# Optimization experiments

Hardware: AMD Instinct MI355X
Metric: run time of the kernel (lower is better)

The kernel has to match this reference:

```python
import jax, jax.numpy as jnp
import numpy as np

EMB = 1024
HEADS = 16
DH = EMB // HEADS
EPS = 1e-5


def _layernorm(x, w, b):
    mean = jnp.mean(x, axis=-1, keepdims=True)
    var = jnp.mean((x - mean) ** 2, axis=-1, keepdims=True)  # unbiased=False
    return w * (x - mean) / jnp.sqrt(var + EPS) + b


def _gelu_tanh(x):
    c = jnp.sqrt(jnp.asarray(2.0 / jnp.pi, x.dtype))
    return 0.5 * x * (1.0 + jnp.tanh(c * (x + 0.044715 * x ** 3)))


def setup_inputs() -> dict:
    key = jax.random.key(0)
    ks = jax.random.split(key, 8)
    B, N = 2, 2048
    s = lambda fan_in: 1.0 / np.sqrt(fan_in)
    # weights stored as [in, out] (torch Linear applied as x @ W.T == x @ W_here)
    return {
        "x": jax.random.normal(ks[0], (B, N, EMB), jnp.float32),
        "ln1_w": jnp.ones((EMB,), jnp.float32),
        "ln1_b": jnp.zeros((EMB,), jnp.float32),
        "w_qkv": jax.random.normal(ks[1], (EMB, 3 * EMB), jnp.float32) * s(EMB),  # qkv_bias=False
        "w_attn_proj": jax.random.normal(ks[2], (EMB, EMB), jnp.float32) * s(EMB),
        "b_attn_proj": jnp.zeros((EMB,), jnp.float32),
        "ln2_w": jnp.ones((EMB,), jnp.float32),
        "ln2_b": jnp.zeros((EMB,), jnp.float32),
        "w_fc": jax.random.normal(ks[3], (EMB, 4 * EMB), jnp.float32) * s(EMB),
        "b_fc": jnp.zeros((4 * EMB,), jnp.float32),
        "w_proj": jax.random.normal(ks[4], (4 * EMB, EMB), jnp.float32) * s(4 * EMB),
        "b_proj": jnp.zeros((EMB,), jnp.float32),
    }


def reference(x, ln1_w, ln1_b, w_qkv, w_attn_proj, b_attn_proj,
              ln2_w, ln2_b, w_fc, b_fc, w_proj, b_proj):
    B, N, _ = x.shape
    # --- attention sublayer (pre-LN) ---
    h = _layernorm(x, ln1_w, ln1_b)
    qkv = h @ w_qkv  # [B,N,3E]
    q, k, v = jnp.split(qkv, 3, axis=-1)
    # [B,H,N,Dh]
    q = q.reshape(B, N, HEADS, DH).transpose(0, 2, 1, 3)
    k = k.reshape(B, N, HEADS, DH).transpose(0, 2, 1, 3)
    v = v.reshape(B, N, HEADS, DH).transpose(0, 2, 1, 3)
    scores = jnp.einsum("bhqd,bhkd->bhqk", q, k) * (DH ** -0.5)
    causal = jnp.tril(jnp.ones((N, N), bool))
    scores = jnp.where(causal, scores, -jnp.inf)
    attn = jax.nn.softmax(scores, axis=-1)  # attn_pdrop=0 (eval)
    ctx = jnp.einsum("bhqk,bhkd->bhqd", attn, v)
    ctx = ctx.transpose(0, 2, 1, 3).reshape(B, N, EMB)
    x = x + (ctx @ w_attn_proj + b_attn_proj)  # resid_pdrop=0
    # --- MLP sublayer (pre-LN) ---
    h = _layernorm(x, ln2_w, ln2_b)
    h = _gelu_tanh(h @ w_fc + b_fc)
    x = x + (h @ w_proj + b_proj)
    return x
```

## Files before the change

### kernel.cpp

```cpp
#include <hip/hip_runtime.h>
#include <stdint.h>

#define EMB 1024
#define NHEAD 16
#define DH 64
#define SEQ 2048
#define NTOK 4096

typedef __attribute__((ext_vector_type(8))) short s16x8;
typedef __attribute__((ext_vector_type(4))) short s16x4;
typedef __attribute__((ext_vector_type(4))) float f32x4;
typedef __attribute__((ext_vector_type(4))) unsigned short u16x4;

__device__ __forceinline__ unsigned short f2bf(float f){
    union { float f; unsigned int u; } v; v.f = f;
    unsigned int r = v.u + 0x7fffu + ((v.u >> 16) & 1u);
    return (unsigned short)(r >> 16);
}

__device__ __forceinline__ f32x4 mfma16(s16x8 a, s16x8 b, f32x4 c){
    return __builtin_amdgcn_mfma_f32_16x16x32_bf16(a, b, c, 0, 0, 0);
}

__device__ __forceinline__ void gload16(const void* g, void* l){
    __builtin_amdgcn_global_load_lds((const __attribute__((address_space(1))) void*)g,
                                     (__attribute__((address_space(3))) void*)l, 16, 0, 0);
}

__device__ __forceinline__ s16x8 cat8(s16x4 a, s16x4 b){
    s16x8 r;
    r[0]=a[0]; r[1]=a[1]; r[2]=a[2]; r[3]=a[3];
    r[4]=b[0]; r[5]=b[1]; r[6]=b[2]; r[7]=b[3];
    return r;
}

__device__ __forceinline__ unsigned cvtpk(float lo, float hi){
    unsigned r;
    asm("v_cvt_pk_bf16_f32 %0, %1, %2" : "=v"(r) : "v"(lo), "v"(hi));
    return r;
}

__device__ __forceinline__ s16x8 qscale(s16x8 q){
    s16x8 r;
    #pragma unroll
    for (int e = 0; e < 8; ++e){
        union { float f; unsigned u; } v;
        v.u = ((unsigned)(unsigned short)q[e]) << 16;
        v.f *= 0.125f;
        r[e] = (short)f2bf(v.f);
    }
    return r;
}

__global__ __launch_bounds__(256) void convT_kernel(const float* __restrict__ in,
                                                    unsigned short* __restrict__ out,
                                                    int R, int C){
    __shared__ float tile[32][33];
    const int c0 = blockIdx.x * 32, r0 = blockIdx.y * 32;
    const int tx = threadIdx.x, ty = threadIdx.y;
    #pragma unroll
    for (int k = 0; k < 4; ++k)
        tile[ty*4+k][tx] = in[(long)(r0 + ty*4 + k) * C + c0 + tx];
    __syncthreads();
    #pragma unroll
    for (int k = 0; k < 4; ++k)
        out[(long)(c0 + ty*4 + k) * R + r0 + tx] = f2bf(tile[tx][ty*4+k]);
}

__global__ __launch_bounds__(256) void vT_kernel(const unsigned short* __restrict__ qkv,
                                                 unsigned short* __restrict__ vtg){
    __shared__ unsigned short tile[64*64];
    const int bh = blockIdx.y, b = bh >> 4, h = bh & 15;
    const int n0 = blockIdx.x * 64;
    const int t = threadIdx.x;
    const int nr = t >> 3, c0 = (t & 7) * 8;
    #pragma unroll
    for (int hh = 0; hh < 2; ++hh){
        const int n = nr + hh*32;
        uint4 vv = *(const uint4*)&qkv[(long)(b*SEQ + n0 + n)*3072 + 2048 + h*64 + c0];
        *(uint4*)((char*)tile + n*128 + ((c0*2) ^ (((n>>3)&7)<<4))) = vv;
    }
    __syncthreads();
    #pragma unroll
    for (int hh = 0; hh < 2; ++hh){
        const int d = nr + hh*32;
        union { unsigned short u[8]; uint4 v; } tmp;
        #pragma unroll
        for (int j = 0; j < 8; ++j){
            const int n = c0 + j;
            tmp.u[j] = *(const unsigned short*)((char*)tile + n*128 + ((d*2) ^ (((n>>3)&7)<<4)));
        }
        *(uint4*)&vtg[((long)bh*64 + d)*2048 + n0 + c0] = tmp.v;
    }
}

__global__ __launch_bounds__(256) void ln_kernel(const float* __restrict__ x,
                                                 const float* __restrict__ w,
                                                 const float* __restrict__ b,
                                                 unsigned short* __restrict__ out){
    const int row = blockIdx.x, tid = threadIdx.x;
    const float4 v = ((const float4*)(x + (long)row * EMB))[tid];
    float s  = v.x + v.y + v.z + v.w;
    float ss = v.x*v.x + v.y*v.y + v.z*v.z + v.w*v.w;
    #pragma unroll
    for (int off = 32; off >= 1; off >>= 1){
        s  += __shfl_xor(s,  off, 64);
        ss += __shfl_xor(ss, off, 64);
    }
    __shared__ float ps[4], pss[4];
    const int wv = tid >> 6;
    if ((tid & 63) == 0){ ps[wv] = s; pss[wv] = ss; }
    __syncthreads();
    s  = ps[0] + ps[1] + ps[2] + ps[3];
    ss = pss[0] + pss[1] + pss[2] + pss[3];
    const float mean = s * (1.0f/EMB);
    const float var  = ss * (1.0f/EMB) - mean*mean;
    const float rstd = rsqrtf(var + 1e-5f);
    const float4 wv4 = ((const float4*)w)[tid];
    const float4 bv4 = ((const float4*)b)[tid];
    u16x4 o;
    o[0] = f2bf((v.x - mean) * rstd * wv4.x + bv4.x);
    o[1] = f2bf((v.y - mean) * rstd * wv4.y + bv4.y);
    o[2] = f2bf((v.z - mean) * rstd * wv4.z + bv4.z);
    o[3] = f2bf((v.w - mean) * rstd * wv4.w + bv4.w);
    *(u16x4*)(out + (long)row * EMB + tid * 4) = o;
}

__global__ __launch_bounds__(256) void red_kernel(const float* __restrict__ p0,
                                                  const float* __restrict__ p1,
                                                  const float* __restrict__ bias,
                                                  const float* __restrict__ resid,
                                                  float* __restrict__ out, int N){
    const long i = ((long)blockIdx.x * 256 + threadIdx.x) * 4;
    const float4 a = *(const float4*)(p0 + i);
    const float4 b = *(const float4*)(p1 + i);
    const float4 r = *(const float4*)(resid + i);
    const float4 bb = *(const float4*)(bias + ((int)i & (N - 1)));
    float4 o;
    o.x = a.x + b.x + r.x + bb.x;
    o.y = a.y + b.y + r.y + bb.y;
    o.z = a.z + b.z + r.z + bb.z;
    o.w = a.w + b.w + r.w + bb.w;
    *(float4*)(out + i) = o;
}

template<int EPI, int SK>
__global__ __launch_bounds__(256, 2) void gemm4_kernel(const unsigned short* __restrict__ A,
                                                       const unsigned short* __restrict__ Bt,
                                                       const float* __restrict__ bias,
                                                       void* __restrict__ out0,
                                                       void* __restrict__ out1,
                                                       int M, int N, int K,
                                                       int xr, int yr){
    __shared__ unsigned short As[2][128*64];
    __shared__ unsigned short Bs[2][128*64];
    const int tid = threadIdx.x, lane = tid & 63, w = tid >> 6;
    const int lm = lane & 15, g = lane >> 4;
    const int wr = w >> 1, wc = w & 1;

    const int gx = gridDim.x;
    const int o = blockIdx.y * gx + blockIdx.x;
    const int x = o & 7, j = o >> 3;
    const int nrx = gx / xr;
    const int m0 = ((x / nrx) * yr + j / xr) * 128;
    const int n0 = ((x % nrx) * xr + j % xr) * 128;
    const int kz = (SK > 1) ? blockIdx.z : 0;
    const int kbase = kz * (K / SK);
    const int nkt = (K / SK) / 64;

    const int r8 = tid >> 3;
    const int src = (((tid & 7) * 16) ^ ((r8 & 7) << 4)) >> 1;
    char* AsB = (char*)&As[0][0];
    char* BsB = (char*)&Bs[0][0];

    auto stage = [&](int bu, int kt){
        #pragma unroll
        for (int p = 0; p < 4; ++p)
            gload16(&A[(long)(m0 + p*32 + r8) * K + kt + src], AsB + bu*16384 + p*4096 + tid*16);
        #pragma unroll
        for (int p = 0; p < 4; ++p)
            gload16(&Bt[(long)(n0 + p*32 + r8) * K + kt + src], BsB + bu*16384 + p*4096 + tid*16);
    };

    f32x4 zero = {0.0f, 0.0f, 0.0f, 0.0f};
    f32x4 acc[4][4];
    #pragma unroll
    for (int i = 0; i < 4; ++i)
        #pragma unroll
        for (int jj = 0; jj < 4; ++jj) acc[i][jj] = zero;

    stage(0, kbase);
    int cur = 0;
    const int axor = (lm & 7) << 4;
    for (int t = 0; t < nkt; ++t){
        if (t + 1 < nkt){
            stage(cur ^ 1, kbase + (t + 1) * 64);
            asm volatile("s_waitcnt vmcnt(8)" ::: "memory");
        } else {
            asm volatile("s_waitcnt vmcnt(0)" ::: "memory");
        }
        __builtin_amdgcn_s_barrier();
        asm volatile("" ::: "memory");
        const char* Ab = AsB + cur*16384;
        const char* Bb = BsB + cur*16384;
        #pragma unroll
        for (int kk = 0; kk < 2; ++kk){
            s16x8 af[4], bf[4];
            #pragma unroll
            for (int i = 0; i < 4; ++i)
                af[i] = *(const s16x8*)(Ab + (wr*64 + i*16 + lm)*128 + ((kk*64 + g*16) ^ axor));
            #pragma unroll
            for (int jj = 0; jj < 4; ++jj)
                bf[jj] = *(const s16x8*)(Bb + (wc*64 + jj*16 + lm)*128 + ((kk*64 + g*16) ^ axor));
            asm volatile("s_waitcnt lgkmcnt(0)" ::: "memory");
            __builtin_amdgcn_sched_barrier(0);
            __builtin_amdgcn_s_setprio(1);
            #pragma unroll
            for (int i = 0; i < 4; ++i)
                #pragma unroll
                for (int jj = 0; jj < 4; ++jj)
                    acc[i][jj] = mfma16(bf[jj], af[i], acc[i][jj]);
            __builtin_amdgcn_s_setprio(0);
        }
        asm volatile("" ::: "memory");
        __builtin_amdgcn_s_barrier();
        asm volatile("" ::: "memory");
        cur ^= 1;
    }

    float* po = (SK > 1 && kz == 1) ? (float*)out1 : (float*)out0;
    #pragma unroll
    for (int i = 0; i < 4; ++i){
        const int row = m0 + wr*64 + i*16 + lm;
        #pragma unroll
        for (int jj = 0; jj < 4; ++jj){
            const int col = n0 + wc*64 + jj*16 + 4*g;
            const f32x4 v = acc[i][jj];
            if (EPI == 0){
                u16x4 ov;
                ov[0] = f2bf(v[0]); ov[1] = f2bf(v[1]);
                ov[2] = f2bf(v[2]); ov[3] = f2bf(v[3]);
                *(u16x4*)&((unsigned short*)out0)[(long)row * N + col] = ov;
            } else if (EPI == 2){
                u16x4 ov;
                #pragma unroll
                for (int r = 0; r < 4; ++r){
                    const float xx = v[r] + bias[col + r];
                    const float z = 0.7978845608f * (xx + 0.044715f * xx * xx * xx);
                    ov[r] = f2bf(xx / (1.0f + __expf(-2.0f * z)));
                }
                *(u16x4*)&((unsigned short*)out0)[(long)row * N + col] = ov;
            } else {
                *(float4*)&po[(long)row * N + col] = *(const float4*)&v;
            }
        }
    }
}

template<int EPI, int BM, int BN, int WR, int WC, int SK>
__global__ __launch_bounds__(WR*WC*64) void gemm_kernel(const unsigned short* __restrict__ A,
                                                        const unsigned short* __restrict__ Bt,
                                                        const float* __restrict__ bias,
                                                        const float* __restrict__ resid,
                                                        void* __restrict__ out0,
                                                        void* __restrict__ out1,
                                                        int M, int N, int K){
    constexpr int NW = WR * WC;
    constexpr int NT = NW * 64;
    constexpr int FI = BM / (WR * 16);
    constexpr int FJ = BN / (WC * 16);
    __shared__ unsigned short As[2][BM * 32];
    __shared__ unsigned short Bs[2][BN * 32];
    const int tid  = threadIdx.x;
    const int lane = tid & 63, w = tid >> 6;
    const int lm = lane & 15, g = lane >> 4;
    const int wr = w / WC, wc = w % WC;

    const int gx = gridDim.x;
    const int nwg = gx * gridDim.y;
    int id = blockIdx.y * gx + blockIdx.x;
    id = (id & 7) * (nwg >> 3) + (id >> 3);
    const int m0 = (id / gx) * BM, n0 = (id % gx) * BN;
    const int kz = (SK > 1) ? blockIdx.z : 0;
    const int kbase = kz * (K / SK);

    f32x4 zero = {0.0f, 0.0f, 0.0f, 0.0f};
    f32x4 acc[FI][FJ];
    #pragma unroll
    for (int i = 0; i < FI; ++i)
        #pragma unroll
        for (int j = 0; j < FJ; ++j) acc[i][j] = zero;

    auto stage = [&](int kt, int bu){
        #pragma unroll
        for (int p = 0; p < BM/(NT/4); ++p)
            gload16(&A[(long)(m0 + p*(NT/4) + (tid>>2)) * K + kt + (tid&3)*8],
                    (char*)&As[bu][0] + p*(NT*16) + tid*16);
        #pragma unroll
        for (int p = 0; p < BN/(NT/4); ++p)
            gload16(&Bt[(long)(n0 + p*(NT/4) + (tid>>2)) * K + kt + (tid&3)*8],
                    (char*)&Bs[bu][0] + p*(NT*16) + tid*16);
    };

    stage(kbase, 0);
    int cur = 0;
    const int nkt = (K / SK) / 32;
    for (int t = 0; t < nkt; ++t){
        __syncthreads();
        if (t + 1 < nkt) stage(kbase + (t+1)*32, cur ^ 1);
        s16x8 af[FI], bf[FJ];
        #pragma unroll
        for (int i = 0; i < FI; ++i)
            af[i] = *(const s16x8*)&As[cur][(wr*(FI*16) + i*16 + lm)*32 + g*8];
        #pragma unroll
        for (int j = 0; j < FJ; ++j)
            bf[j] = *(const s16x8*)&Bs[cur][(wc*(FJ*16) + j*16 + lm)*32 + g*8];
        #pragma unroll
        for (int i = 0; i < FI; ++i)
            #pragma unroll
            for (int j = 0; j < FJ; ++j)
                acc[i][j] = mfma16(af[i], bf[j], acc[i][j]);
        cur ^= 1;
    }

    float* po = (SK > 1 && kz == 1) ? (float*)out1 : (float*)out0;
    #pragma unroll
    for (int i = 0; i < FI; ++i){
        #pragma unroll
        for (int r = 0; r < 4; ++r){
            const int row = m0 + wr*(FI*16) + i*16 + 4*g + r;
            #pragma unroll
            for (int j = 0; j < FJ; ++j){
                const int col = n0 + wc*(FJ*16) + j*16 + lm;
                const float v = acc[i][j][r];
                if (EPI == 0){
                    ((unsigned short*)out0)[(long)row * N + col] = f2bf(v);
                } else if (EPI == 1){
                    ((float*)out0)[(long)row * N + col] =
                        v + bias[col] + resid[(long)row * N + col];
                } else if (EPI == 2){
                    const float xx = v + bias[col];
                    const float z = 0.7978845608f * (xx + 0.044715f * xx * xx * xx);
                    const float gg = xx / (1.0f + __expf(-2.0f * z));
                    ((unsigned short*)out0)[(long)row * N + col] = f2bf(gg);
                } else {
                    po[(long)row * N + col] = v;
                }
            }
        }
    }
}

__global__ __launch_bounds__(256) void attn_kernel(const unsigned short* __restrict__ qkv,
                                                   const unsigned short* __restrict__ vtg,
                                                   unsigned short* __restrict__ ctx){
    __shared__ unsigned short Ks[3][4096];
    __shared__ unsigned short Vs[3][4096];
    int id0 = blockIdx.y * 16 + blockIdx.x;
    const int id = (id0 & 7) * 64 + (id0 >> 3);
    const int pair = id & 15, bh = id >> 4;
    const int b = bh >> 4, h = bh & 15;
    const int tid = threadIdx.x, lane = tid & 63, w = tid >> 6;
    const int lm = lane & 15, g = lane >> 4;
    const long qkvb = (long)b * SEQ * 3072;
    const unsigned short* kglob = qkv + qkvb + 1024 + h*64;
    const unsigned short* vglob = vtg + (long)bh * 64 * 2048;

    const int srow = tid >> 3;
    const int soff = (tid & 7) * 16;
    const int swz = (lm & 7) << 4;
    f32x4 zero = {0.0f, 0.0f, 0.0f, 0.0f};

    #pragma unroll 1
    for (int grp = 0; grp < 2; ++grp){
        const int qg = (grp == 0) ? pair : (31 - pair);
        const int q0 = qg * 64;
        const int nt = qg + 1;
        const int qrow = q0 + w*16 + lm;

        const unsigned short* qrp = qkv + qkvb + (long)qrow*3072 + h*64;
        const s16x8 qf0 = qscale(*(const s16x8*)(qrp + g*8));
        const s16x8 qf1 = qscale(*(const s16x8*)(qrp + 32 + g*8));

        f32x4 o[4];
        #pragma unroll
        for (int d = 0; d < 4; ++d) o[d] = zero;
        float lsum = 0.0f;

        auto stageKV = [&](int t, int bu){
            const int kv0 = t * 64;
            #pragma unroll
            for (int hh = 0; hh < 2; ++hh){
                const int row = srow + hh*32;
                const int sw  = soff ^ ((row & 7) << 4);
                gload16(kglob + (long)(kv0 + row)*3072 + (sw >> 1),
                        (char*)&Ks[bu][0] + hh*4096 + w*1024);
                gload16(vglob + (long)row*2048 + kv0 + (sw >> 1),
                        (char*)&Vs[bu][0] + hh*4096 + w*1024);
            }
        };
        auto qkt = [&](int bu, f32x4* sc){
            const char* Kb = (const char*)&Ks[bu][0];
            #pragma unroll
            for (int s = 0; s < 4; ++s){
                const char* rp = Kb + (s*16 + lm)*128;
                s16x8 kf0 = *(const s16x8*)(rp + ((g*16) ^ swz));
                s16x8 kf1 = *(const s16x8*)(rp + ((64 + g*16) ^ swz));
                f32x4 a = mfma16(kf0, qf0, zero);
                sc[s] = mfma16(kf1, qf1, a);
            }
        };

        __builtin_amdgcn_s_barrier();
        asm volatile("" ::: "memory");
        stageKV(0, 0);
        if (nt > 1){
            stageKV(1, 1);
            asm volatile("s_waitcnt vmcnt(4)" ::: "memory");
        } else {
            asm volatile("s_waitcnt vmcnt(0)" ::: "memory");
        }
        __builtin_amdgcn_s_barrier();
        asm volatile("" ::: "memory");

        f32x4 sc[4], scN[4];
        qkt(0, sc);

        #pragma unroll 1
        for (int t = 0; t < nt; ++t){
            const bool more = (t + 1 < nt);
            if (more){
                asm volatile("s_waitcnt vmcnt(0)" ::: "memory");
                __builtin_amdgcn_s_barrier();
                asm volatile("" ::: "memory");
                if (t + 2 < nt) stageKV(t + 2, (t + 2) % 3);
                qkt((t + 1) % 3, scN);
            }

            if (t == nt - 1){
                #pragma unroll
                for (int s = 0; s < 4; ++s)
                    #pragma unroll
                    for (int r = 0; r < 4; ++r)
                        if (s*16 + 4*g + r > w*16 + lm) sc[s][r] = -1e30f;
            }
            float pp[4][4];
            #pragma unroll
            for (int s = 0; s < 4; ++s)
                #pragma unroll
                for (int r = 0; r < 4; ++r){
                    const float e = __expf(sc[s][r]);
                    pp[s][r] = e;
                    lsum += e;
                }

            union { unsigned u[4]; s16x8 v; } P0, P1;
            P0.u[0] = cvtpk(pp[0][0], pp[0][1]);
            P0.u[1] = cvtpk(pp[0][2], pp[0][3]);
            P0.u[2] = cvtpk(pp[1][0], pp[1][1]);
            P0.u[3] = cvtpk(pp[1][2], pp[1][3]);
            P1.u[0] = cvtpk(pp[2][0], pp[2][1]);
            P1.u[1] = cvtpk(pp[2][2], pp[2][3]);
            P1.u[2] = cvtpk(pp[3][0], pp[3][1]);
            P1.u[3] = cvtpk(pp[3][2], pp[3][3]);

            const char* Vb = (const char*)&Vs[t % 3][0];
            #pragma unroll
            for (int d = 0; d < 4; ++d){
                const char* vrp = Vb + (d*16 + lm)*128;
                s16x4 a0 = *(const s16x4*)(vrp + ((g*8) ^ swz));
                s16x4 a1 = *(const s16x4*)(vrp + ((32 + g*8) ^ swz));
                o[d] = mfma16(cat8(a0, a1), P0.v, o[d]);
                s16x4 b0 = *(const s16x4*)(vrp + ((64 + g*8) ^ swz));
                s16x4 b1 = *(const s16x4*)(vrp + ((96 + g*8) ^ swz));
                o[d] = mfma16(cat8(b0, b1), P1.v, o[d]);
            }
            if (more){
                #pragma unroll
                for (int s4 = 0; s4 < 4; ++s4) sc[s4] = scN[s4];
            }
        }

        lsum += __shfl_xor(lsum, 16, 64);
        lsum += __shfl_xor(lsum, 32, 64);
        const float inv = 1.0f / lsum;
        unsigned short* cw = ctx + (long)(b*SEQ + qrow)*EMB + h*DH + 4*g;
        #pragma unroll
        for (int d = 0; d < 4; ++d){
            u16x4 ov;
            ov[0] = f2bf(o[d][0]*inv); ov[1] = f2bf(o[d][1]*inv);
            ov[2] = f2bf(o[d][2]*inv); ov[3] = f2bf(o[d][3]*inv);
            *(u16x4*)(cw + d*16) = ov;
        }
    }
}

extern "C" void kernel_launch(void* const* d_in, const int* in_sizes, int n_in,
                              void* d_out, int out_size, void* d_ws, size_t ws_size,
                              hipStream_t stream){
    const float* x     = (const float*)d_in[0];
    const float* ln1_w = (const float*)d_in[1];
    const float* ln1_b = (const float*)d_in[2];
    const float* w_qkv = (const float*)d_in[3];
    const float* w_ap  = (const float*)d_in[4];
    const float* b_ap  = (const float*)d_in[5];
    const float* ln2_w = (const float*)d_in[6];
    const float* ln2_b = (const float*)d_in[7];
    const float* w_fc  = (const float*)d_in[8];
    const float* b_fc  = (const float*)d_in[9];
    const float* w_pr  = (const float*)d_in[10];
    const float* b_pr  = (const float*)d_in[11];
    float* out = (float*)d_out;

    char* ws = (char*)d_ws;
    unsigned short* wqkvT = (unsigned short*)(ws + 0);
    unsigned short* wapT  = (unsigned short*)(ws + 6291456);
    unsigned short* wfcT  = (unsigned short*)(ws + 8388608);
    unsigned short* wprT  = (unsigned short*)(ws + 16777216);
    unsigned short* h1    = (unsigned short*)(ws + 25165824);
    unsigned short* vtg   = (unsigned short*)(ws + 25165824);
    unsigned short* qkv   = (unsigned short*)(ws + 33554432);
    unsigned short* ctx   = (unsigned short*)(ws + 58720256);
    float*          x1    = (float*)(ws + 67108864);
    unsigned short* h2    = (unsigned short*)(ws + 83886080);
    unsigned short* afc   = (unsigned short*)(ws + 92274688);
    float* pp0 = (float*)(ws + 0);
    float* pp1 = (float*)(ws + 25165824);

    dim3 b32(32, 8, 1);
    convT_kernel<<<dim3(3072/32, 1024/32), b32, 0, stream>>>(w_qkv, wqkvT, 1024, 3072);
    convT_kernel<<<dim3(1024/32, 1024/32), b32, 0, stream>>>(w_ap,  wapT,  1024, 1024);
    convT_kernel<<<dim3(4096/32, 1024/32), b32, 0, stream>>>(w_fc,  wfcT,  1024, 4096);
    convT_kernel<<<dim3(1024/32, 4096/32), b32, 0, stream>>>(w_pr,  wprT,  4096, 1024);

    ln_kernel<<<NTOK, 256, 0, stream>>>(x, ln1_w, ln1_b, h1);

    gemm4_kernel<0,1><<<dim3(3072/128, NTOK/128), 256, 0, stream>>>(
        h1, wqkvT, nullptr, qkv, nullptr, NTOK, 3072, 1024, 12, 8);

    vT_kernel<<<dim3(SEQ/64, 32), 256, 0, stream>>>(qkv, vtg);

    attn_kernel<<<dim3(16, 32), 256, 0, stream>>>(qkv, vtg, ctx);

    gemm_kernel<1,128,64,2,2,1><<<dim3(1024/64, NTOK/128), 256, 0, stream>>>(
        ctx, wapT, b_ap, x, x1, nullptr, NTOK, 1024, 1024);

    ln_kernel<<<NTOK, 256, 0, stream>>>(x1, ln2_w, ln2_b, h2);

    gemm4_kernel<2,1><<<dim3(4096/128, NTOK/128), 256, 0, stream>>>(
        h2, wfcT, b_fc, afc, nullptr, NTOK, 4096, 1024, 16, 8);

    gemm4_kernel<3,2><<<dim3(1024/128, NTOK/128, 2), 256, 0, stream>>>(
        afc, wprT, nullptr, pp0, pp1, NTOK, 1024, 4096, 8, 4);
    red_kernel<<<NTOK*EMB/1024, 256, 0, stream>>>(pp0, pp1, b_pr, x1, out, EMB);
}
```

Measured before the change: 241.2 us.

## Replace split-K proj GEMM and old attn-proj GEMM with fused 128x64 kernel

Adds a new 128x64-tile GEMM kernel that uses the swizzled 64-wide K staging, with bias and residual fused into its epilogue. It is used for both the attention output projection and the MLP down-projection. This drops the split-K partial buffers and the separate reduction kernel, and replaces the older 32-K-step GEMM. The four weight-transpose launches are also merged into one kernel. The MLP projection loses split-K parallelism but gets more blocks through the smaller N tile and an occupancy hint of 3.

```diff
diff --git a/kernel.cpp b/kernel.cpp
--- a/kernel.cpp
+++ b/kernel.cpp
@@ -52,11 +52,18 @@
     return r;
 }
 
-__global__ __launch_bounds__(256) void convT_kernel(const float* __restrict__ in,
-                                                    unsigned short* __restrict__ out,
-                                                    int R, int C){
+__global__ __launch_bounds__(256) void convT4_kernel(const float* __restrict__ q, unsigned short* __restrict__ qo,
+                                                     const float* __restrict__ a, unsigned short* __restrict__ ao,
+                                                     const float* __restrict__ f, unsigned short* __restrict__ fo,
+                                                     const float* __restrict__ p, unsigned short* __restrict__ po){
     __shared__ float tile[32][33];
-    const int c0 = blockIdx.x * 32, r0 = blockIdx.y * 32;
+    int id = blockIdx.x;
+    const float* in; unsigned short* out; int R, C, bx, by;
+    if (id < 3072)      { in = q; out = qo; R = 1024; C = 3072; bx = id % 96;  by = id / 96;  }
+    else if (id < 4096) { id -= 3072; in = a; out = ao; R = 1024; C = 1024; bx = id % 32; by = id / 32; }
+    else if (id < 8192) { id -= 4096; in = f; out = fo; R = 1024; C = 4096; bx = id % 128; by = id / 128; }
+    else                { id -= 8192; in = p; out = po; R = 4096; C = 1024; bx = id % 32; by = id / 32; }
+    const int c0 = bx * 32, r0 = by * 32;
     const int tx = threadIdx.x, ty = threadIdx.y;
     #pragma unroll
     for (int k = 0; k < 4; ++k)
@@ -126,30 +133,11 @@
     *(u16x4*)(out + (long)row * EMB + tid * 4) = o;
 }
 
-__global__ __launch_bounds__(256) void red_kernel(const float* __restrict__ p0,
-                                                  const float* __restrict__ p1,
-                                                  const float* __restrict__ bias,
-                                                  const float* __restrict__ resid,
-                                                  float* __restrict__ out, int N){
-    const long i = ((long)blockIdx.x * 256 + threadIdx.x) * 4;
-    const float4 a = *(const float4*)(p0 + i);
-    const float4 b = *(const float4*)(p1 + i);
-    const float4 r = *(const float4*)(resid + i);
-    const float4 bb = *(const float4*)(bias + ((int)i & (N - 1)));
-    float4 o;
-    o.x = a.x + b.x + r.x + bb.x;
-    o.y = a.y + b.y + r.y + bb.y;
-    o.z = a.z + b.z + r.z + bb.z;
-    o.w = a.w + b.w + r.w + bb.w;
-    *(float4*)(out + i) = o;
-}
-
-template<int EPI, int SK>
+template<int EPI>
 __global__ __launch_bounds__(256, 2) void gemm4_kernel(const unsigned short* __restrict__ A,
                                                        const unsigned short* __restrict__ Bt,
                                                        const float* __restrict__ bias,
                                                        void* __restrict__ out0,
-                                                       void* __restrict__ out1,
                                                        int M, int N, int K,
                                                        int xr, int yr){
     __shared__ unsigned short As[2][128*64];
@@ -164,9 +152,7 @@
     const int nrx = gx / xr;
     const int m0 = ((x / nrx) * yr + j / xr) * 128;
     const int n0 = ((x % nrx) * xr + j % xr) * 128;
-    const int kz = (SK > 1) ? blockIdx.z : 0;
-    const int kbase = kz * (K / SK);
-    const int nkt = (K / SK) / 64;
+    const int nkt = K / 64;
 
     const int r8 = tid >> 3;
     const int src = (((tid & 7) * 16) ^ ((r8 & 7) << 4)) >> 1;
@@ -189,12 +175,12 @@
         #pragma unroll
         for (int jj = 0; jj < 4; ++jj) acc[i][jj] = zero;
 
-    stage(0, kbase);
+    stage(0, 0);
     int cur = 0;
     const int axor = (lm & 7) << 4;
     for (int t = 0; t < nkt; ++t){
         if (t + 1 < nkt){
-            stage(cur ^ 1, kbase + (t + 1) * 64);
+            stage(cur ^ 1, (t + 1) * 64);
             asm volatile("s_waitcnt vmcnt(8)" ::: "memory");
         } else {
             asm volatile("s_waitcnt vmcnt(0)" ::: "memory");
@@ -228,7 +214,6 @@
         cur ^= 1;
     }
 
-    float* po = (SK > 1 && kz == 1) ? (float*)out1 : (float*)out0;
     #pragma unroll
     for (int i = 0; i < 4; ++i){
         const int row = m0 + wr*64 + i*16 + lm;
@@ -241,7 +226,7 @@
                 ov[0] = f2bf(v[0]); ov[1] = f2bf(v[1]);
                 ov[2] = f2bf(v[2]); ov[3] = f2bf(v[3]);
                 *(u16x4*)&((unsigned short*)out0)[(long)row * N + col] = ov;
-            } else if (EPI == 2){
+            } else {
                 u16x4 ov;
                 #pragma unroll
                 for (int r = 0; r < 4; ++r){
@@ -250,103 +235,107 @@
                     ov[r] = f2bf(xx / (1.0f + __expf(-2.0f * z)));
                 }
                 *(u16x4*)&((unsigned short*)out0)[(long)row * N + col] = ov;
-            } else {
-                *(float4*)&po[(long)row * N + col] = *(const float4*)&v;
-            }
-        }
-    }
-}
-
-template<int EPI, int BM, int BN, int WR, int WC, int SK>
-__global__ __launch_bounds__(WR*WC*64) void gemm_kernel(const unsigned short* __restrict__ A,
-                                                        const unsigned short* __restrict__ Bt,
-                                                        const float* __restrict__ bias,
-                                                        const float* __restrict__ resid,
-                                                        void* __restrict__ out0,
-                                                        void* __restrict__ out1,
-                                                        int M, int N, int K){
-    constexpr int NW = WR * WC;
-    constexpr int NT = NW * 64;
-    constexpr int FI = BM / (WR * 16);
-    constexpr int FJ = BN / (WC * 16);
-    __shared__ unsigned short As[2][BM * 32];
-    __shared__ unsigned short Bs[2][BN * 32];
-    const int tid  = threadIdx.x;
-    const int lane = tid & 63, w = tid >> 6;
+            }
+        }
+    }
+}
+
+__global__ __launch_bounds__(256, 3) void gemm5_kernel(const unsigned short* __restrict__ A,
+                                                       const unsigned short* __restrict__ Bt,
+                                                       const float* __restrict__ bias,
+                                                       const float* __restrict__ resid,
+                                                       float* __restrict__ out0,
+                                                       int M, int N, int K,
+                                                       int xr, int yr){
+    __shared__ unsigned short As[2][128*64];
+    __shared__ unsigned short Bs[2][64*64];
+    const int tid = threadIdx.x, lane = tid & 63, w = tid >> 6;
     const int lm = lane & 15, g = lane >> 4;
-    const int wr = w / WC, wc = w % WC;
+    const int wr = w >> 1, wc = w & 1;
 
     const int gx = gridDim.x;
-    const int nwg = gx * gridDim.y;
-    int id = blockIdx.y * gx + blockIdx.x;
-    id = (id & 7) * (nwg >> 3) + (id >> 3);
-    const int m0 = (id / gx) * BM, n0 = (id % gx) * BN;
-    const int kz = (SK > 1) ? blockIdx.z : 0;
-    const int kbase = kz * (K / SK);
+    const int o = blockIdx.y * gx + blockIdx.x;
+    const int x = o & 7, j = o >> 3;
+    const int nrx = gx / xr;
+    const int m0 = ((x / nrx) * yr + j / xr) * 128;
+    const int n0 = ((x % nrx) * xr + j % xr) * 64;
+    const int nkt = K / 64;
+
+    const int r8 = tid >> 3;
+    const int src = (((tid & 7) * 16) ^ ((r8 & 7) << 4)) >> 1;
+    char* AsB = (char*)&As[0][0];
+    char* BsB = (char*)&Bs[0][0];
+
+    auto stage = [&](int bu, int kt){
+        #pragma unroll
+        for (int p = 0; p < 4; ++p)
+            gload16(&A[(long)(m0 + p*32 + r8) * K + kt + src], AsB + bu*16384 + p*4096 + tid*16);
+        #pragma unroll
+        for (int p = 0; p < 2; ++p)
+            gload16(&Bt[(long)(n0 + p*32 + r8) * K + kt + src], BsB + bu*8192 + p*4096 + tid*16);
+    };
 
     f32x4 zero = {0.0f, 0.0f, 0.0f, 0.0f};
-    f32x4 acc[FI][FJ];
-    #pragma unroll
-    for (int i = 0; i < FI; ++i)
-        #pragma unroll
-        for (int j = 0; j < FJ; ++j) acc[i][j] = zero;
-
-    auto stage = [&](int kt, int bu){
-        #pragma unroll
-        for (int p = 0; p < BM/(NT/4); ++p)
-            gload16(&A[(long)(m0 + p*(NT/4) + (tid>>2)) * K + kt + (tid&3)*8],
-                    (char*)&As[bu][0] + p*(NT*16) + tid*16);
-        #pragma unroll
-        for (int p = 0; p < BN/(NT/4); ++p)
-            gload16(&Bt[(long)(n0 + p*(NT/4) + (tid>>2)) * K + kt + (tid&3)*8],
-                    (char*)&Bs[bu][0] + p*(NT*16) + tid*16);
-    };
-
-    stage(kbase, 0);
+    f32x4 acc[4][2];
+    #pragma unroll
+    for (int i = 0; i < 4; ++i)
+        #pragma unroll
+        for (int jj = 0; jj < 2; ++jj) acc[i][jj] = zero;
+
+    stage(0, 0);
     int cur = 0;
-    const int nkt = (K / SK) / 32;
+    const int axor = (lm & 7) << 4;
     for (int t = 0; t < nkt; ++t){
-        __syncthreads();
-        if (t + 1 < nkt) stage(kbase + (t+1)*32, cur ^ 1);
-        s16x8 af[FI], bf[FJ];
-        #pragma unroll
-        for (int i = 0; i < FI; ++i)
-            af[i] = *(const s16x8*)&As[cur][(wr*(FI*16) + i*16 + lm)*32 + g*8];
-        #pragma unroll
-        for (int j = 0; j < FJ; ++j)
-            bf[j] = *(const s16x8*)&Bs[cur][(wc*(FJ*16) + j*16 + lm)*32 + g*8];
-        #pragma unroll
-        for (int i = 0; i < FI; ++i)
-            #pragma unroll
-            for (int j = 0; j < FJ; ++j)
-                acc[i][j] = mfma16(af[i], bf[j], acc[i][j]);
+        if (t + 1 < nkt){
+            stage(cur ^ 1, (t + 1) * 64);
+            asm volatile("s_waitcnt vmcnt(6)" ::: "memory");
+        } else {
+            asm volatile("s_waitcnt vmcnt(0)" ::: "memory");
+        }
+        __builtin_amdgcn_s_barrier();
+        asm volatile("" ::: "memory");
+        const char* Ab = AsB + cur*16384;
+        const char* Bb = BsB + cur*8192;
+        #pragma unroll
+        for (int kk = 0; kk < 2; ++kk){
+            s16x8 af[4], bf[2];
+            #pragma unroll
+            for (int i = 0; i < 4; ++i)
+                af[i] = *(const s16x8*)(Ab + (wr*64 + i*16 + lm)*128 + ((kk*64 + g*16) ^ axor));
+            #pragma unroll
+            for (int jj = 0; jj < 2; ++jj)
+                bf[jj] = *(const s16x8*)(Bb + (wc*32 + jj*16 + lm)*128 + ((kk*64 + g*16) ^ axor));
+            asm volatile("s_waitcnt lgkmcnt(0)" ::: "memory");
+            __builtin_amdgcn_sched_barrier(0);
+            __builtin_amdgcn_s_setprio(1);
+            #pragma unroll
+            for (int i = 0; i < 4; ++i)
+                #pragma unroll
+                for (int jj = 0; jj < 2; ++jj)
+                    acc[i][jj] = mfma16(bf[jj], af[i], acc[i][jj]);
+            __builtin_amdgcn_s_setprio(0);
+        }
+        asm volatile("" ::: "memory");
+        __builtin_amdgcn_s_barrier();
+        asm volatile("" ::: "memory");
         cur ^= 1;
     }
 
-    float* po = (SK > 1 && kz == 1) ? (float*)out1 : (float*)out0;
-    #pragma unroll
-    for (int i = 0; i < FI; ++i){
-        #pragma unroll
-        for (int r = 0; r < 4; ++r){
-            const int row = m0 + wr*(FI*16) + i*16 + 4*g + r;
-            #pragma unroll
-            for (int j = 0; j < FJ; ++j){
-                const int col = n0 + wc*(FJ*16) + j*16 + lm;
-                const float v = acc[i][j][r];
-                if (EPI == 0){
-                    ((unsigned short*)out0)[(long)row * N + col] = f2bf(v);
-                } else if (EPI == 1){
-                    ((float*)out0)[(long)row * N + col] =
-                        v + bias[col] + resid[(long)row * N + col];
-                } else if (EPI == 2){
-                    const float xx = v + bias[col];
-                    const float z = 0.7978845608f * (xx + 0.044715f * xx * xx * xx);
-                    const float gg = xx / (1.0f + __expf(-2.0f * z));
-                    ((unsigned short*)out0)[(long)row * N + col] = f2bf(gg);
-                } else {
-                    po[(long)row * N + col] = v;
-                }
-            }
+    #pragma unroll
+    for (int i = 0; i < 4; ++i){
+        const int row = m0 + wr*64 + i*16 + lm;
+        #pragma unroll
+        for (int jj = 0; jj < 2; ++jj){
+            const int col = n0 + wc*32 + jj*16 + 4*g;
+            const f32x4 v = acc[i][jj];
+            const float4 bb = *(const float4*)&bias[col];
+            const float4 rr = *(const float4*)&resid[(long)row * N + col];
+            float4 ov;
+            ov.x = v[0] + bb.x + rr.x;
+            ov.y = v[1] + bb.y + rr.y;
+            ov.z = v[2] + bb.z + rr.z;
+            ov.w = v[3] + bb.w + rr.w;
+            *(float4*)&out0[(long)row * N + col] = ov;
         }
     }
 }
@@ -524,33 +513,27 @@
     float*          x1    = (float*)(ws + 67108864);
     unsigned short* h2    = (unsigned short*)(ws + 83886080);
     unsigned short* afc   = (unsigned short*)(ws + 92274688);
-    float* pp0 = (float*)(ws + 0);
-    float* pp1 = (float*)(ws + 25165824);
-
-    dim3 b32(32, 8, 1);
-    convT_kernel<<<dim3(3072/32, 1024/32), b32, 0, stream>>>(w_qkv, wqkvT, 1024, 3072);
-    convT_kernel<<<dim3(1024/32, 1024/32), b32, 0, stream>>>(w_ap,  wapT,  1024, 1024);
-    convT_kernel<<<dim3(4096/32, 1024/32), b32, 0, stream>>>(w_fc,  wfcT,  1024, 4096);
-    convT_kernel<<<dim3(1024/32, 4096/32), b32, 0, stream>>>(w_pr,  wprT,  4096, 1024);
+
+    convT4_kernel<<<12288, dim3(32, 8, 1), 0, stream>>>(
+        w_qkv, wqkvT, w_ap, wapT, w_fc, wfcT, w_pr, wprT);
 
     ln_kernel<<<NTOK, 256, 0, stream>>>(x, ln1_w, ln1_b, h1);
 
-    gemm4_kernel<0,1><<<dim3(3072/128, NTOK/128), 256, 0, stream>>>(
-        h1, wqkvT, nullptr, qkv, nullptr, NTOK, 3072, 1024, 12, 8);
+    gemm4_kernel<0><<<dim3(3072/128, NTOK/128), 256, 0, stream>>>(
+        h1, wqkvT, nullptr, qkv, NTOK, 3072, 1024, 12, 8);
 
     vT_kernel<<<dim3(SEQ/64, 32), 256, 0, stream>>>(qkv, vtg);
 
     attn_kernel<<<dim3(16, 32), 256, 0, stream>>>(qkv, vtg, ctx);
 
-    gemm_kernel<1,128,64,2,2,1><<<dim3(1024/64, NTOK/128), 256, 0, stream>>>(
-        ctx, wapT, b_ap, x, x1, nullptr, NTOK, 1024, 1024);
+    gemm5_kernel<<<dim3(1024/64, NTOK/128), 256, 0, stream>>>(
+        ctx, wapT, b_ap, x, x1, NTOK, 1024, 1024, 8, 8);
 
     ln_kernel<<<NTOK, 256, 0, stream>>>(x1, ln2_w, ln2_b, h2);
 
-    gemm4_kernel<2,1><<<dim3(4096/128, NTOK/128), 256, 0, stream>>>(
-        h2, wfcT, b_fc, afc, nullptr, NTOK, 4096, 1024, 16, 8);
-
-    gemm4_kernel<3,2><<<dim3(1024/128, NTOK/128, 2), 256, 0, stream>>>(
-        afc, wprT, nullptr, pp0, pp1, NTOK, 1024, 4096, 8, 4);
-    red_kernel<<<NTOK*EMB/1024, 256, 0, stream>>>(pp0, pp1, b_pr, x1, out, EMB);
-}
+    gemm4_kernel<2><<<dim3(4096/128, NTOK/128), 256, 0, stream>>>(
+        h2, wfcT, b_fc, afc, NTOK, 4096, 1024, 16, 8);
+
+    gemm5_kernel<<<dim3(1024/64, NTOK/128), 256, 0, stream>>>(
+        afc, wprT, b_pr, x1, out, NTOK, 1024, 4096, 8, 8);
+}
```

Measured after the change: 238.6 us. Within noise of the previous version (-1.1%).
